# Performance work log

Hardware: AMD Instinct MI355X
Metric: run time of the kernel (lower is better)

Reference implementation:

```python
import jax, jax.numpy as jnp
import numpy as np

# Brevitas-style fake quantization:
#  - Int8ActPerTensorFloat: signed, symmetric, per-tensor float scale, range [-128, 127]
#  - 4-bit weight, narrow range: [-7, 7]
#  - Int32Bias: quantized at scale s_in * s_w
# Scales are taken from per-tensor abs-max statistics (brevitas stats-based init).

def _round(v):
    return jnp.round(v)

def _fake_quant(v, scale, qmin, qmax):
    return jnp.clip(_round(v / scale), qmin, qmax) * scale


def setup_inputs() -> dict:
    key = jax.random.key(0)
    k1, k2, k3 = jax.random.split(key, 3)
    x = jax.random.normal(k1, (16, 3, 224, 224), dtype=jnp.float32)
    W = jax.random.normal(k2, (128, 3, 3, 3), dtype=jnp.float32) * 0.1
    b = jax.random.normal(k3, (128,), dtype=jnp.float32) * 0.01
    return {"x": x, "W": W, "b": b}


def reference(x, W, b):
    EPS = 1e-8
    # input quant: int8 per-tensor
    s_in = jnp.maximum(jnp.max(jnp.abs(x)) / 127.0, EPS)
    x_q = _fake_quant(x, s_in, -128.0, 127.0)
    # weight quant: 4-bit narrow-range per-tensor
    s_w = jnp.maximum(jnp.max(jnp.abs(W)) / 7.0, EPS)
    w_q = _fake_quant(W, s_w, -7.0, 7.0)
    # bias quant: int32 at scale s_in * s_w
    s_b = s_in * s_w
    b_q = _fake_quant(b, s_b, -2147483648.0, 2147483647.0)
    # conv2d, NCHW x OIHW -> NCHW, stride 1, valid padding (torch default padding=0)
    y = jax.lax.conv_general_dilated(
        x_q, w_q, window_strides=(1, 1), padding="VALID",
        dimension_numbers=("NCHW", "OIHW", "NCHW"))
    y = y + b_q[None, :, None, None]
    # output quant: int8 per-tensor
    s_out = jnp.maximum(jnp.max(jnp.abs(y)) / 127.0, EPS)
    y_q = _fake_quant(y, s_out, -128.0, 127.0)
    return y_q
```

## Files before the change

kernel.cpp:

```cpp
#include <hip/hip_runtime.h>
#include <stdint.h>

#define QEPS 1e-8f

typedef __bf16 bf16x8 __attribute__((ext_vector_type(8)));
typedef unsigned short ushortx8 __attribute__((ext_vector_type(8)));
typedef float floatx4 __attribute__((ext_vector_type(4)));


__global__ void k_init(unsigned int* s) { if (threadIdx.x < 4) s[threadIdx.x] = 0u; }

__global__ __launch_bounds__(256) void k_absmax(
    const float4* __restrict__ x, int n4,
    const float* __restrict__ W, int nw,
    unsigned int* __restrict__ s) {
  __shared__ unsigned int red[256];
  const int t = threadIdx.x;
  unsigned int m = 0u;
  const int i = blockIdx.x * 256 + t;
  if (i < n4) {
    float4 v = x[i];
    m =        __float_as_uint(v.x) & 0x7fffffffu;
    m = max(m, __float_as_uint(v.y) & 0x7fffffffu);
    m = max(m, __float_as_uint(v.z) & 0x7fffffffu);
    m = max(m, __float_as_uint(v.w) & 0x7fffffffu);
  }
  red[t] = m;
  __syncthreads();
  for (int off = 128; off > 0; off >>= 1) {
    if (t < off) red[t] = max(red[t], red[t + off]);
    __syncthreads();
  }
  if (t == 0) atomicMax(&s[0], red[0]);

  if (blockIdx.x == 0) {
    unsigned int mw = 0u;
    for (int j = t; j < nw; j += 256)
      mw = max(mw, __float_as_uint(W[j]) & 0x7fffffffu);
    __syncthreads();
    red[t] = mw;
    __syncthreads();
    for (int off = 128; off > 0; off >>= 1) {
      if (t < off) red[t] = max(red[t], red[t + off]);
      __syncthreads();
    }
    if (t == 0) atomicMax(&s[1], red[0]);
  }
}

template<int PASS>
__global__ __launch_bounds__(256) void k_conv(
    const float* __restrict__ x, const float* __restrict__ W,
    const float* __restrict__ b, float* __restrict__ out,
    unsigned int* __restrict__ s) {
  __shared__ __align__(16) unsigned short wl[32 * 130];
  __shared__ __align__(16) unsigned short xl[19 * 228];
  __shared__ __align__(16) float qbl[128];
  __shared__ float redf[256];

  const int t = threadIdx.x;
  const float s_in = fmaxf(__uint_as_float(s[0]) / 127.0f, QEPS);
  const float s_w  = fmaxf(__uint_as_float(s[1]) / 7.0f,  QEPS);
  const float s_b  = s_in * s_w;

  float s_out = 1.0f, h = 1.0f;
  if (PASS == 1) {
    const float vmax = __uint_as_float(s[2]);
    s_out = fmaxf((s_b * vmax) / 127.0f, QEPS);
    h = s_b / s_out;
  }

  for (int i = t; i < 3456; i += 256) {
    const int o = i / 27;
    const int k = i - o * 27;
    float q = rintf(W[i] / s_w);
    q = fminf(fmaxf(q, -7.0f), 7.0f);
    wl[k * 130 + o] = (unsigned short)(__float_as_uint(q) >> 16);
  }
  for (int i = t; i < 5 * 130; i += 256) wl[27 * 130 + i] = 0;

  if (t < 128) qbl[t] = rintf(b[t] / s_b);

  for (int i = t; i < 72; i += 256) {
    const int r = i >> 2;
    xl[r * 228 + 224 + (i & 3)] = 0;
  }
  for (int i = t; i < 228; i += 256) xl[18 * 228 + i] = 0;

  #pragma unroll
  for (int sl = 0; sl < 2; ++sl) {
    const int R = blockIdx.x + sl * 1776;
    const int n = R / 222, oh = R - n * 222;
    for (int i = t; i < 9 * 224; i += 256) {
      const int row = i / 224;
      const int col = i - row * 224;
      const int c = row / 3, kh = row - c * 3;
      const float xv = x[((n * 3 + c) * 224 + (oh + kh)) * 224 + col];
      float q = fminf(fmaxf(rintf(xv / s_in), -128.0f), 127.0f);
      xl[(sl * 9 + row) * 228 + col] = (unsigned short)(__float_as_uint(q) >> 16);
    }
  }
  __syncthreads();

  const int lane = t & 63;
  const int wv = t >> 6;
  const int p = lane & 15;
  const int g = lane >> 4;

  bf16x8 av[8];
  #pragma unroll
  for (int tt8 = 0; tt8 < 8; ++tt8) {
    ushortx8 u;
    #pragma unroll
    for (int j = 0; j < 8; ++j)
      u[j] = wl[(g * 8 + j) * 130 + tt8 * 16 + p];
    av[tt8] = __builtin_bit_cast(bf16x8, u);
  }

  float vmax_local = 0.0f;

  #pragma unroll
  for (int sl = 0; sl < 2; ++sl) {
    int off2[8];
    #pragma unroll
    for (int j = 0; j < 8; ++j) {
      const int k = g * 8 + j;
      int row, kw;
      if (k < 27) {
        const int c = k / 9, rem = k - c * 9;
        const int kh = rem / 3;
        kw = rem - kh * 3;
        row = sl * 9 + c * 3 + kh;
      } else { row = 18; kw = 0; }
      off2[j] = (row * 228 + kw) * 2;
    }

    const int R = blockIdx.x + sl * 1776;
    const int nn = R / 222, ohh = R - nn * 222;
    const int tt0 = sl * 14;
    const int start = tt0 + ((wv - tt0) & 3);

    #pragma unroll 1
    for (int tt = start; tt < tt0 + 14; tt += 4) {
      const int ow0 = (tt - tt0) * 16;
      const char* xbase = (const char*)xl + (ow0 + p) * 2;

      ushortx8 bu;
      #pragma unroll
      for (int j = 0; j < 8; ++j)
        bu[j] = *(const unsigned short*)(xbase + off2[j]);
      const bf16x8 bv = __builtin_bit_cast(bf16x8, bu);

      floatx4 acc[8];
      #pragma unroll
      for (int tt8 = 0; tt8 < 8; ++tt8)
        acc[tt8] = *(const floatx4*)&qbl[tt8 * 16 + g * 4];
      #pragma unroll
      for (int tt8 = 0; tt8 < 8; ++tt8)
        acc[tt8] = __builtin_amdgcn_mfma_f32_16x16x32_bf16(av[tt8], bv, acc[tt8], 0, 0, 0);

      const int ow = ow0 + p;
      if (PASS == 0) {
        if (ow < 222) {
          #pragma unroll
          for (int tt8 = 0; tt8 < 8; ++tt8)
            #pragma unroll
            for (int r = 0; r < 4; ++r)
              vmax_local = fmaxf(vmax_local, fabsf(acc[tt8][r]));
        }
      } else {
        if (ow < 222) {
          float* ob = out + ((nn * 128 + g * 4) * 222 + ohh) * 222 + ow;
          #pragma unroll
          for (int tt8 = 0; tt8 < 8; ++tt8) {
            #pragma unroll
            for (int r = 0; r < 4; ++r) {
              float q = rintf(acc[tt8][r] * h);
              q = fminf(fmaxf(q, -128.0f), 127.0f);
              ob[(tt8 * 16 + r) * 49284] = q * s_out;
            }
          }
        }
      }
    }
  }

  if (PASS == 0) {
    redf[t] = vmax_local;
    __syncthreads();
    for (int off = 128; off > 0; off >>= 1) {
      if (t < off) redf[t] = fmaxf(redf[t], redf[t + off]);
      __syncthreads();
    }
    if (t == 0) atomicMax(&s[2], __float_as_uint(redf[0]));
  }
}

extern "C" void kernel_launch(void* const* d_in, const int* in_sizes, int n_in,
                              void* d_out, int out_size, void* d_ws, size_t ws_size,
                              hipStream_t stream) {
  const float* x = (const float*)d_in[0];
  const float* W = (const float*)d_in[1];
  const float* b = (const float*)d_in[2];
  float* out = (float*)d_out;
  unsigned int* s = (unsigned int*)d_ws;

  k_init<<<1, 64, 0, stream>>>(s);

  const int n4 = in_sizes[0] / 4;
  k_absmax<<<(n4 + 255) / 256, 256, 0, stream>>>(
      (const float4*)x, n4, W, in_sizes[1], s);

  k_conv<0><<<1776, 256, 0, stream>>>(x, W, b, out, s);
  k_conv<1><<<1776, 256, 0, stream>>>(x, W, b, out, s);
}
```

Before: 591.5 us.

## Stage quantized output as packed int8 in LDS for coalesced float4 stores

```diff
diff --git a/kernel.cpp b/kernel.cpp
--- a/kernel.cpp
+++ b/kernel.cpp
@@ -48,15 +48,24 @@
   }
 }
 
+#define OFF_XL  8320
+#define OFF_QBL 16992
+#define OFF_RED 17504
+#define OFF_OL  18528
+#define SMEM_P0 18528
+#define SMEM_P1 47712
+
 template<int PASS>
 __global__ __launch_bounds__(256) void k_conv(
     const float* __restrict__ x, const float* __restrict__ W,
     const float* __restrict__ b, float* __restrict__ out,
     unsigned int* __restrict__ s) {
-  __shared__ __align__(16) unsigned short wl[32 * 130];
-  __shared__ __align__(16) unsigned short xl[19 * 228];
-  __shared__ __align__(16) float qbl[128];
-  __shared__ float redf[256];
+  extern __shared__ __align__(16) char smem[];
+  unsigned short* const wl   = (unsigned short*)smem;
+  unsigned short* const xl   = (unsigned short*)(smem + OFF_XL);
+  float*          const qbl  = (float*)(smem + OFF_QBL);
+  float*          const redf = (float*)(smem + OFF_RED);
+  unsigned int*   const ol32 = (unsigned int*)(smem + OFF_OL);
 
   const int t = threadIdx.x;
   const float s_in = fmaxf(__uint_as_float(s[0]) / 127.0f, QEPS);
@@ -78,13 +87,8 @@
     wl[k * 130 + o] = (unsigned short)(__float_as_uint(q) >> 16);
   }
   for (int i = t; i < 5 * 130; i += 256) wl[27 * 130 + i] = 0;
-
   if (t < 128) qbl[t] = rintf(b[t] / s_b);
-
-  for (int i = t; i < 72; i += 256) {
-    const int r = i >> 2;
-    xl[r * 228 + 224 + (i & 3)] = 0;
-  }
+  for (int i = t; i < 72; i += 256) xl[(i >> 2) * 228 + 224 + (i & 3)] = 0;
   for (int i = t; i < 228; i += 256) xl[18 * 228 + i] = 0;
 
   #pragma unroll
@@ -107,15 +111,18 @@
   const int p = lane & 15;
   const int g = lane >> 4;
 
-  bf16x8 av[8];
+  bf16x8 bvw[8];
   #pragma unroll
   for (int tt8 = 0; tt8 < 8; ++tt8) {
     ushortx8 u;
     #pragma unroll
     for (int j = 0; j < 8; ++j)
       u[j] = wl[(g * 8 + j) * 130 + tt8 * 16 + p];
-    av[tt8] = __builtin_bit_cast(bf16x8, u);
-  }
+    bvw[tt8] = __builtin_bit_cast(bf16x8, u);
+  }
+  float qbp[8];
+  #pragma unroll
+  for (int tt8 = 0; tt8 < 8; ++tt8) qbp[tt8] = qbl[tt8 * 16 + p];
 
   float vmax_local = 0.0f;
 
@@ -137,51 +144,83 @@
 
     const int R = blockIdx.x + sl * 1776;
     const int nn = R / 222, ohh = R - nn * 222;
-    const int tt0 = sl * 14;
-    const int start = tt0 + ((wv - tt0) & 3);
 
     #pragma unroll 1
-    for (int tt = start; tt < tt0 + 14; tt += 4) {
-      const int ow0 = (tt - tt0) * 16;
+    for (int tt = wv; tt < 14; tt += 4) {
+      const int ow0 = tt * 16;
       const char* xbase = (const char*)xl + (ow0 + p) * 2;
 
       ushortx8 bu;
       #pragma unroll
       for (int j = 0; j < 8; ++j)
         bu[j] = *(const unsigned short*)(xbase + off2[j]);
-      const bf16x8 bv = __builtin_bit_cast(bf16x8, bu);
+      const bf16x8 av = __builtin_bit_cast(bf16x8, bu);
 
       floatx4 acc[8];
       #pragma unroll
-      for (int tt8 = 0; tt8 < 8; ++tt8)
-        acc[tt8] = *(const floatx4*)&qbl[tt8 * 16 + g * 4];
+      for (int tt8 = 0; tt8 < 8; ++tt8) {
+        const float qb = qbp[tt8];
+        acc[tt8][0] = qb; acc[tt8][1] = qb; acc[tt8][2] = qb; acc[tt8][3] = qb;
+      }
       #pragma unroll
       for (int tt8 = 0; tt8 < 8; ++tt8)
-        acc[tt8] = __builtin_amdgcn_mfma_f32_16x16x32_bf16(av[tt8], bv, acc[tt8], 0, 0, 0);
-
-      const int ow = ow0 + p;
+        acc[tt8] = __builtin_amdgcn_mfma_f32_16x16x32_bf16(av, bvw[tt8], acc[tt8], 0, 0, 0);
+
       if (PASS == 0) {
-        if (ow < 222) {
+        #pragma unroll
+        for (int tt8 = 0; tt8 < 8; ++tt8)
           #pragma unroll
-          for (int tt8 = 0; tt8 < 8; ++tt8)
-            #pragma unroll
-            for (int r = 0; r < 4; ++r)
-              vmax_local = fmaxf(vmax_local, fabsf(acc[tt8][r]));
+          for (int r = 0; r < 4; ++r)
+            vmax_local = fmaxf(vmax_local,
+                (ow0 + 4 * g + r < 222) ? fabsf(acc[tt8][r]) : 0.0f);
+      } else {
+        #pragma unroll
+        for (int tt8 = 0; tt8 < 8; ++tt8) {
+          unsigned int pk = 0;
+          #pragma unroll
+          for (int r = 0; r < 4; ++r) {
+            float q = rintf(acc[tt8][r] * h);
+            q = fminf(fmaxf(q, -128.0f), 127.0f);
+            pk |= ((unsigned int)((int)q & 255)) << (8 * r);
+          }
+          ol32[(tt8 * 16 + p) * 57 + (ow0 >> 2) + g] = pk;
         }
-      } else {
-        if (ow < 222) {
-          float* ob = out + ((nn * 128 + g * 4) * 222 + ohh) * 222 + ow;
-          #pragma unroll
-          for (int tt8 = 0; tt8 < 8; ++tt8) {
-            #pragma unroll
-            for (int r = 0; r < 4; ++r) {
-              float q = rintf(acc[tt8][r] * h);
-              q = fminf(fmaxf(q, -128.0f), 127.0f);
-              ob[(tt8 * 16 + r) * 49284] = q * s_out;
+      }
+    }
+
+    if (PASS == 1) {
+      __syncthreads();
+      #pragma unroll 1
+      for (int oc = wv * 32; oc < wv * 32 + 32; ++oc) {
+        const unsigned int* src = ol32 + oc * 57;
+        float* dst = out + (((nn * 128 + oc) * 222 + ohh) * 222);
+        if (lane < 56) {
+          const unsigned int bc = src[lane];
+          if ((ohh & 1) == 0) {
+            float f0 = (float)((int)(bc << 24) >> 24) * s_out;
+            float f1 = (float)((int)(bc << 16) >> 24) * s_out;
+            float f2 = (float)((int)(bc <<  8) >> 24) * s_out;
+            float f3 = (float)((int) bc        >> 24) * s_out;
+            if (lane < 55) *(float4*)(dst + 4 * lane) = make_float4(f0, f1, f2, f3);
+            else           *(float2*)(dst + 220)      = make_float2(f0, f1);
+          } else {
+            if (lane == 0) {
+              float f0 = (float)((int)(bc << 24) >> 24) * s_out;
+              float f1 = (float)((int)(bc << 16) >> 24) * s_out;
+              *(float2*)dst = make_float2(f0, f1);
+            } else {
+              const unsigned int ap = src[lane - 1];
+              const unsigned int v = (ap >> 16) | (bc << 16);
+              float f0 = (float)((int)(v << 24) >> 24) * s_out;
+              float f1 = (float)((int)(v << 16) >> 24) * s_out;
+              float f2 = (float)((int)(v <<  8) >> 24) * s_out;
+              float f3 = (float)((int) v        >> 24) * s_out;
+              *(float4*)(dst + 4 * lane - 2) = make_float4(f0, f1, f2, f3);
             }
           }
         }
       }
+      __syncthreads();
     }
   }
 
@@ -211,6 +250,6 @@
   k_absmax<<<(n4 + 255) / 256, 256, 0, stream>>>(
       (const float4*)x, n4, W, in_sizes[1], s);
 
-  k_conv<0><<<1776, 256, 0, stream>>>(x, W, b, out, s);
-  k_conv<1><<<1776, 256, 0, stream>>>(x, W, b, out, s);
+  k_conv<0><<<1776, 256, SMEM_P0, stream>>>(x, W, b, out, s);
+  k_conv<1><<<1776, 256, SMEM_P1, stream>>>(x, W, b, out, s);
 }
```

Result: faster. 574.1 us (-2.9%).
